# Kernel optimization log

Measured on AMD Instinct MI355X. Metric: run time of the kernel, lower is better.

## Reference

```python
import jax, jax.numpy as jnp
import numpy as np

D_MODEL = 2048
NUM_HEADS = 16
HEAD_DIM = D_MODEL // NUM_HEADS
SCALE = HEAD_DIM ** 0.5
B, TQ, CACHE_LEN = 4, 1024, 1024


def setup_inputs() -> dict:
    key = jax.random.key(0)
    ks = jax.random.split(key, 13)
    f = jnp.float32
    inp = {
        'query': jax.random.normal(ks[0], (B, TQ, D_MODEL), f),
        'key': jax.random.normal(ks[1], (B, TQ, D_MODEL), f),
        'value': jax.random.normal(ks[2], (B, TQ, D_MODEL), f),
        'cache_key': jax.random.normal(ks[3], (B, CACHE_LEN, D_MODEL), f),
        'cache_value': jax.random.normal(ks[4], (B, CACHE_LEN, D_MODEL), f),
        'Wq': jax.random.normal(ks[5], (D_MODEL, D_MODEL), f) * 0.02,
        'bq': jnp.zeros((D_MODEL,), f),
        'Wk': jax.random.normal(ks[6], (D_MODEL, D_MODEL), f) * 0.02,
        'bk': jnp.zeros((D_MODEL,), f),
        'Wv': jax.random.normal(ks[7], (D_MODEL, D_MODEL), f) * 0.02,
        'bv': jnp.zeros((D_MODEL,), f),
        'Wo': jax.random.normal(ks[8], (D_MODEL, D_MODEL), f) * 0.02,
        'bo': jnp.zeros((D_MODEL,), f),
    }
    return inp


def _split(x):
    b, t, _ = x.shape
    return jnp.transpose(x.reshape(b, t, NUM_HEADS, HEAD_DIM), (0, 2, 1, 3))  # [B,H,T,Dh]


def reference(query, key, value, cache_key, cache_value, Wq, bq, Wk, bk, Wv, bv, Wo, bo):
    b, tq, _ = query.shape
    Q = query @ Wq.T + bq
    K = key @ Wk.T + bk
    V = value @ Wv.T + bv
    # cache holds already-projected K/V; concat along time
    K = jnp.concatenate([cache_key, K], axis=1)
    V = jnp.concatenate([cache_value, V], axis=1)
    total = K.shape[1]
    Qh, Kh, Vh = _split(Q), _split(K), _split(V)  # [B,H,T,Dh]
    scores = jnp.einsum('bhqd,bhkd->bhqk', Qh, Kh) / SCALE  # [B,H,Tq,total]
    # faithful to original: tril(Tq, total) mask (row i sees cols 0..i)
    mask = jnp.tril(jnp.ones((tq, total), dtype=bool))
    scores = jnp.where(mask[None, None], scores, -jnp.inf)
    attn = jax.nn.softmax(scores, axis=-1)  # eval mode: no dropout
    out = jnp.einsum('bhqk,bhkd->bhqd', attn, Vh)
    out = jnp.transpose(out, (0, 2, 1, 3)).reshape(b, tq, D_MODEL)
    out = out @ Wo.T + bo
    # new cache: torch reshapes the transposed [B,H,T,Dh] tensor directly
    new_k = Kh.reshape(b, -1, D_MODEL)
    new_v = Vh.reshape(b, -1, D_MODEL)
    return out, new_k, new_v
```

## Files before the change

### kernel.cpp

```cpp
#include <hip/hip_runtime.h>
#include <hip/hip_bf16.h>


typedef __bf16 bf16x8 __attribute__((ext_vector_type(8)));
typedef __bf16 bf16x4 __attribute__((ext_vector_type(4)));
typedef unsigned short u16x8 __attribute__((ext_vector_type(8)));
typedef float  f32x4  __attribute__((ext_vector_type(4)));
typedef unsigned int u32;

#define MFMA16(a, b, c) __builtin_amdgcn_mfma_f32_16x16x32_bf16((a), (b), (c), 0, 0, 0)

__device__ __forceinline__ void async16(__bf16* lds, const __bf16* g) {
    __builtin_amdgcn_global_load_lds(
        (__attribute__((address_space(1))) void*)g,
        (__attribute__((address_space(3))) void*)lds, 16, 0, 0);
}

__global__ __launch_bounds__(256) void cvt_all(
    const float* __restrict__ q, const float* __restrict__ k, const float* __restrict__ v,
    const float* __restrict__ wq, const float* __restrict__ wk,
    const float* __restrict__ wv, const float* __restrict__ wo,
    __bf16* __restrict__ dq, __bf16* __restrict__ dk, __bf16* __restrict__ dv,
    __bf16* __restrict__ dwq, __bf16* __restrict__ dwk,
    __bf16* __restrict__ dwv, __bf16* __restrict__ dwo) {
    const int nthreads = gridDim.x * blockDim.x;
    for (int i = blockIdx.x * blockDim.x + threadIdx.x; i < 5242880; i += nthreads) {
        const float* s;
        __bf16* d;
        int off;
        if (i < (3 << 20)) {
            const int r = i >> 20;
            off = i & ((1 << 20) - 1);
            s = (r == 0) ? q : (r == 1) ? k : v;
            d = (r == 0) ? dq : (r == 1) ? dk : dv;
        } else {
            const int j = i - (3 << 20);
            const int r = j >> 19;
            off = j & ((1 << 19) - 1);
            s = (r == 0) ? wq : (r == 1) ? wk : (r == 2) ? wv : wo;
            d = (r == 0) ? dwq : (r == 1) ? dwk : (r == 2) ? dwv : dwo;
        }
        const f32x4 x0 = *(const f32x4*)(s + (size_t)off * 8);
        const f32x4 x1 = *(const f32x4*)(s + (size_t)off * 8 + 4);
        bf16x8 o;
#pragma unroll
        for (int j = 0; j < 4; j++) {
            o[j]     = (__bf16)x0[j];
            o[j + 4] = (__bf16)x1[j];
        }
        *(bf16x8*)(d + (size_t)off * 8) = o;
    }
}

template <int MODE>
__global__ __launch_bounds__(256) void gemm_bf(const __bf16* __restrict__ A,
                                               const __bf16* __restrict__ W,
                                               const float* __restrict__ bias,
                                               void* __restrict__ Cv) {
    constexpr int K = 2048;
    __shared__ __bf16 aT[128 * 32];
    __shared__ __bf16 bT[128 * 32];

    float* Cf = (float*)Cv;
    __bf16* Cb = (__bf16*)Cv;

    const int tid = threadIdx.x;
    const int w = tid >> 6;
    const int lane = tid & 63;

    const int lin = (blockIdx.y << 4) | blockIdx.x;
    const int swz = ((lin & 7) << 6) | (lin >> 3);
    const int m0 = (swz >> 4) << 7;
    const int n0 = (swz & 15) << 7;

    const int wr = w >> 1, wc = w & 1;
    const int g = lane >> 4, c = lane & 15;

    const int srow = w * 32 + (lane >> 2);
    const int kch = (lane & 3) * 8;
    const __bf16* gA0 = A + (size_t)(m0 + srow) * K + kch;
    const __bf16* gB0 = W + (size_t)(n0 + srow) * K + kch;
    __bf16* lA0 = &aT[w * 1024];
    __bf16* lB0 = &bT[w * 1024];

    f32x4 acc[4][4] = {};
    const int arow = wr * 64 + c;
    const int brow = wc * 64 + c;
    const int koff = g * 8;

    for (int k0 = 0; k0 < K; k0 += 32) {
        async16(lA0,       gA0 + k0);
        async16(lA0 + 512, gA0 + 16 * K + k0);
        async16(lB0,       gB0 + k0);
        async16(lB0 + 512, gB0 + 16 * K + k0);
        __syncthreads();
        bf16x8 af[4], bfr[4];
#pragma unroll
        for (int t = 0; t < 4; t++) {
            af[t]  = *(const bf16x8*)&aT[(arow + t * 16) * 32 + koff];
            bfr[t] = *(const bf16x8*)&bT[(brow + t * 16) * 32 + koff];
        }
#pragma unroll
        for (int ti = 0; ti < 4; ti++)
#pragma unroll
            for (int tj = 0; tj < 4; tj++)
                acc[ti][tj] = MFMA16(af[ti], bfr[tj], acc[ti][tj]);
        __syncthreads();
    }

#pragma unroll
    for (int tj = 0; tj < 4; tj++) {
        const int gcol = n0 + wc * 64 + tj * 16 + c;
        const float bv = bias[gcol];
#pragma unroll
        for (int ti = 0; ti < 4; ti++) {
            const int growb = m0 + wr * 64 + ti * 16 + g * 4;
#pragma unroll
            for (int r = 0; r < 4; r++) {
                const float v = acc[ti][tj][r] + bv;
                const int row = growb + r;
                if (MODE == 0) {
                    Cf[(size_t)row * 2048 + gcol] = v;
                } else {
                    const int b = row >> 10, t = row & 1023;
                    const int h = gcol >> 7, dh = gcol & 127;
                    if (MODE == 1)
                        Cb[(((size_t)(b * 16 + h) * 1024) + t) * 128 + dh] = (__bf16)v;
                    else
                        Cf[(((size_t)(b * 16 + h) * 2048) + 1024 + t) * 128 + dh] = v;
                }
            }
        }
    }
}

__global__ __launch_bounds__(256) void copy_cache(const float* __restrict__ ck,
                                                  const float* __restrict__ cv,
                                                  float* __restrict__ nk,
                                                  float* __restrict__ nv,
                                                  __bf16* __restrict__ ckb,
                                                  __bf16* __restrict__ cvb) {
    const int nthreads = gridDim.x * blockDim.x;
    for (int i = blockIdx.x * blockDim.x + threadIdx.x; i < 4194304; i += nthreads) {
        const int sel = i >> 21;
        const int j = i & 2097151;
        const int dh4 = j & 31;
        const int t = (j >> 5) & 1023;
        const int h = (j >> 15) & 15;
        const int b = j >> 19;
        const float* src = sel ? cv : ck;
        float* dst = sel ? nv : nk;
        __bf16* dstb = sel ? cvb : ckb;
        const size_t si = ((size_t)(b << 10) + t) * 2048 + (h << 7) + (dh4 << 2);
        const size_t di = ((size_t)b << 22) + ((size_t)h << 18) + (t << 7) + (dh4 << 2);
        const f32x4 x = *(const f32x4*)&src[si];
        *(f32x4*)&dst[di] = x;
        bf16x4 bx;
#pragma unroll
        for (int e = 0; e < 4; e++) bx[e] = (__bf16)x[e];
        *(bf16x4*)&dstb[si] = bx;
    }
}

__global__ __launch_bounds__(256) void attn_k(const __bf16* __restrict__ Qw,
                                              const __bf16* __restrict__ cK,
                                              const __bf16* __restrict__ cV,
                                              __bf16* __restrict__ O) {
    __shared__ __bf16 Kt[32 * 128];
    __shared__ u32 Vt32[128 * 16];
    __shared__ __bf16 Pw[4][16 * 32];

    const int tid = threadIdx.x;
    const int w = tid >> 6;
    const int lane = tid & 63;
    const int g = lane >> 4, c = lane & 15;

    const int lin = blockIdx.x + (blockIdx.y << 4) + (blockIdx.z << 8);
    const int chunk = lin >> 8, idx = lin & 255;
    int qb = idx & 15;
    if (chunk & 1) qb = 15 - qb;
    const int bh = (idx >> 4) + (chunk << 4);
    const int b = bh >> 4, h = bh & 15;
    const int q0 = qb << 6;
    const float inv_scale = 0.08838834764831845f;

    const __bf16* qbase = Qw + (((size_t)(b * 16 + h) * 1024) + q0 + w * 16) * 128;
    bf16x8 qf[4];
#pragma unroll
    for (int dc = 0; dc < 4; dc++)
        qf[dc] = *(const bf16x8*)&qbase[c * 128 + dc * 32 + g * 8];

    f32x4 accO[8] = {};
    float m_run[4], l_run[4];
#pragma unroll
    for (int r = 0; r < 4; r++) { m_run[r] = -1e30f; l_run[r] = 0.0f; }

    const int trips = (q0 >> 5) + 2;
    const __bf16* kb = cK + (size_t)b * 1024 * 2048 + h * 128;
    const __bf16* vb = cV + (size_t)b * 1024 * 2048 + h * 128;

    const int skey = tid >> 3, sdh = (tid & 7) * 16;
    const int kp = tid >> 4, db = tid & 15;
    const int vcol = (((kp >> 2) ^ (db & 3)) << 2) | (kp & 3);

    for (int kt = 0; kt < trips; kt++) {
        const int k0 = kt * 32;
        const bf16x8 k_lo = *(const bf16x8*)&kb[(size_t)(k0 + skey) * 2048 + sdh];
        const bf16x8 k_hi = *(const bf16x8*)&kb[(size_t)(k0 + skey) * 2048 + sdh + 8];
        const bf16x8 v0 = *(const bf16x8*)&vb[(size_t)(k0 + 2 * kp) * 2048 + db * 8];
        const bf16x8 v1 = *(const bf16x8*)&vb[(size_t)(k0 + 2 * kp + 1) * 2048 + db * 8];
        __syncthreads();
        {
            const int ss = skey & 7, ch0 = (tid & 7) * 2;
            *(bf16x8*)&Kt[skey * 128 + ((ch0 ^ ss) << 3)]       = k_lo;
            *(bf16x8*)&Kt[skey * 128 + (((ch0 + 1) ^ ss) << 3)] = k_hi;
        }
        {
            const u16x8 pa = __builtin_bit_cast(u16x8, v0);
            const u16x8 pb = __builtin_bit_cast(u16x8, v1);
#pragma unroll
            for (int j = 0; j < 8; j++)
                Vt32[(db * 8 + j) * 16 + vcol] = (u32)pa[j] | ((u32)pb[j] << 16);
        }
        __syncthreads();

        f32x4 s_acc[2] = {};
#pragma unroll
        for (int nt = 0; nt < 2; nt++) {
            const int krow = nt * 16 + c;
            const int ks = krow & 7;
#pragma unroll
            for (int dc = 0; dc < 4; dc++) {
                const bf16x8 kf =
                    *(const bf16x8*)&Kt[krow * 128 + (((dc * 4 + g) ^ ks) << 3)];
                s_acc[nt] = MFMA16(qf[dc], kf, s_acc[nt]);
            }
        }

        float p[2][4], alpha[4];
#pragma unroll
        for (int r = 0; r < 4; r++) {
            const int qrow = q0 + w * 16 + g * 4 + r;
            float s0 = (k0 + c      <= qrow) ? s_acc[0][r] * inv_scale : -1e30f;
            float s1 = (k0 + 16 + c <= qrow) ? s_acc[1][r] * inv_scale : -1e30f;
            float rm = fmaxf(s0, s1);
            rm = fmaxf(rm, __shfl_xor(rm, 1));
            rm = fmaxf(rm, __shfl_xor(rm, 2));
            rm = fmaxf(rm, __shfl_xor(rm, 4));
            rm = fmaxf(rm, __shfl_xor(rm, 8));
            const float mnew = fmaxf(m_run[r], rm);
            alpha[r] = __expf(m_run[r] - mnew);
            const float p0 = __expf(s0 - mnew);
            const float p1 = __expf(s1 - mnew);
            p[0][r] = p0; p[1][r] = p1;
            float ps = p0 + p1;
            ps += __shfl_xor(ps, 1);
            ps += __shfl_xor(ps, 2);
            ps += __shfl_xor(ps, 4);
            ps += __shfl_xor(ps, 8);
            l_run[r] = alpha[r] * l_run[r] + ps;
            m_run[r] = mnew;
        }
#pragma unroll
        for (int nt2 = 0; nt2 < 8; nt2++)
#pragma unroll
            for (int r = 0; r < 4; r++)
                accO[nt2][r] *= alpha[r];

#pragma unroll
        for (int nt = 0; nt < 2; nt++)
#pragma unroll
            for (int r = 0; r < 4; r++)
                Pw[w][(g * 4 + r) * 32 + ((((nt << 1) | (c >> 3)) ^ g) << 3) + (c & 7)] =
                    (__bf16)p[nt][r];
        __syncthreads();

        const bf16x8 pf = *(const bf16x8*)&Pw[w][c * 32 + ((g ^ ((c >> 2) & 3)) << 3)];
#pragma unroll
        for (int nt2 = 0; nt2 < 8; nt2++) {
            const int vrow = nt2 * 16 + c;
            const bf16x8 vf = *(const bf16x8*)&(
                (const __bf16*)Vt32)[vrow * 32 + ((g ^ ((vrow >> 3) & 3)) << 3)];
            accO[nt2] = MFMA16(pf, vf, accO[nt2]);
        }
    }

#pragma unroll
    for (int nt2 = 0; nt2 < 8; nt2++)
#pragma unroll
        for (int r = 0; r < 4; r++) {
            const float v = accO[nt2][r] / l_run[r];
            const int row = b * 1024 + q0 + w * 16 + g * 4 + r;
            const int col = h * 128 + nt2 * 16 + c;
            O[(size_t)row * 2048 + col] = (__bf16)v;
        }
}

extern "C" void kernel_launch(void* const* d_in, const int* in_sizes, int n_in,
                              void* d_out, int out_size, void* d_ws, size_t ws_size,
                              hipStream_t stream) {
    const float* query       = (const float*)d_in[0];
    const float* key         = (const float*)d_in[1];
    const float* value       = (const float*)d_in[2];
    const float* cache_key   = (const float*)d_in[3];
    const float* cache_value = (const float*)d_in[4];
    const float* Wq = (const float*)d_in[5];
    const float* bq = (const float*)d_in[6];
    const float* Wk = (const float*)d_in[7];
    const float* bk = (const float*)d_in[8];
    const float* Wv = (const float*)d_in[9];
    const float* bv = (const float*)d_in[10];
    const float* Wo = (const float*)d_in[11];
    const float* bo = (const float*)d_in[12];

    float* out   = (float*)d_out;
    float* new_k = out + 8388608;
    float* new_v = out + 25165824;

    __bf16* p = (__bf16*)d_ws;
    __bf16* ws_q    = p; p += 8388608;
    __bf16* ws_attn = p; p += 8388608;
    __bf16* q_bf    = p; p += 8388608;
    __bf16* k_bf    = p; p += 8388608;
    __bf16* v_bf    = p; p += 8388608;
    __bf16* wq_bf   = p; p += 4194304;
    __bf16* wk_bf   = p; p += 4194304;
    __bf16* wv_bf   = p; p += 4194304;
    __bf16* wo_bf   = p; p += 4194304;
    __bf16* ck_bf   = p; p += 8388608;
    __bf16* cv_bf   = p;

    const dim3 gemm_grid(16, 32);

    copy_cache<<<4096, 256, 0, stream>>>(cache_key, cache_value, new_k, new_v,
                                         ck_bf, cv_bf);
    cvt_all<<<2048, 256, 0, stream>>>(query, key, value, Wq, Wk, Wv, Wo,
                                      q_bf, k_bf, v_bf, wq_bf, wk_bf, wv_bf, wo_bf);
    gemm_bf<1><<<gemm_grid, 256, 0, stream>>>(q_bf, wq_bf, bq, ws_q);
    gemm_bf<2><<<gemm_grid, 256, 0, stream>>>(k_bf, wk_bf, bk, new_k);
    gemm_bf<2><<<gemm_grid, 256, 0, stream>>>(v_bf, wv_bf, bv, new_v);
    attn_k<<<dim3(16, 16, 4), 256, 0, stream>>>(ws_q, ck_bf, cv_bf, ws_attn);
    gemm_bf<0><<<gemm_grid, 256, 0, stream>>>(ws_attn, wo_bf, bo, out);
}
```

Baseline: 650.6 us.

## Fuse prep kernels, batch QKV GEMMs, widen attention key tile

The cache copy and the fp32-to-bf16 conversion kernels are merged into one prep kernel, which now also writes the bf16 cache in head-major layout. The three QKV projection GEMMs become a single launch that picks its weight, bias and output per row segment; this relies on q_bf, k_bf and v_bf sitting contiguously in the workspace. The attention kernel moves to 64-key tiles, loads K asynchronously straight into LDS from the contiguous head-major cache, and replaces the block barrier before the per-wave P buffer read with an LDS waitcnt. The aim is fewer launches, better GPU fill and fewer barriers, at the cost of more LDS per block and a dependence on workspace layout.

```diff
diff --git a/kernel.cpp b/kernel.cpp
--- a/kernel.cpp
+++ b/kernel.cpp
@@ -16,62 +16,90 @@
         (__attribute__((address_space(3))) void*)lds, 16, 0, 0);
 }
 
-__global__ __launch_bounds__(256) void cvt_all(
+__global__ __launch_bounds__(256) void prep(
     const float* __restrict__ q, const float* __restrict__ k, const float* __restrict__ v,
     const float* __restrict__ wq, const float* __restrict__ wk,
     const float* __restrict__ wv, const float* __restrict__ wo,
+    const float* __restrict__ ck, const float* __restrict__ cv,
+    float* __restrict__ nk, float* __restrict__ nv,
     __bf16* __restrict__ dq, __bf16* __restrict__ dk, __bf16* __restrict__ dv,
     __bf16* __restrict__ dwq, __bf16* __restrict__ dwk,
-    __bf16* __restrict__ dwv, __bf16* __restrict__ dwo) {
+    __bf16* __restrict__ dwv, __bf16* __restrict__ dwo,
+    __bf16* __restrict__ ckb, __bf16* __restrict__ cvb) {
     const int nthreads = gridDim.x * blockDim.x;
-    for (int i = blockIdx.x * blockDim.x + threadIdx.x; i < 5242880; i += nthreads) {
-        const float* s;
-        __bf16* d;
-        int off;
-        if (i < (3 << 20)) {
-            const int r = i >> 20;
-            off = i & ((1 << 20) - 1);
-            s = (r == 0) ? q : (r == 1) ? k : v;
-            d = (r == 0) ? dq : (r == 1) ? dk : dv;
+    for (int i = blockIdx.x * blockDim.x + threadIdx.x; i < 9437184; i += nthreads) {
+        if (i < 4194304) {
+            const int sel = i >> 21;
+            const int j = i & 2097151;
+            const int dh4 = j & 31;
+            const int t = (j >> 5) & 1023;
+            const int h = (j >> 15) & 15;
+            const int b = j >> 19;
+            const float* src = sel ? cv : ck;
+            float* dst = sel ? nv : nk;
+            __bf16* dstb = sel ? cvb : ckb;
+            const size_t si = ((size_t)(b << 10) + t) * 2048 + (h << 7) + (dh4 << 2);
+            const size_t di = ((size_t)b << 22) + ((size_t)h << 18) + (t << 7) + (dh4 << 2);
+            const size_t bi = (((size_t)(b * 16 + h) * 1024 + t) << 7) + (dh4 << 2);
+            const f32x4 x = *(const f32x4*)&src[si];
+            *(f32x4*)&dst[di] = x;
+            bf16x4 bx;
+#pragma unroll
+            for (int e = 0; e < 4; e++) bx[e] = (__bf16)x[e];
+            *(bf16x4*)&dstb[bi] = bx;
         } else {
-            const int j = i - (3 << 20);
-            const int r = j >> 19;
-            off = j & ((1 << 19) - 1);
-            s = (r == 0) ? wq : (r == 1) ? wk : (r == 2) ? wv : wo;
-            d = (r == 0) ? dwq : (r == 1) ? dwk : (r == 2) ? dwv : dwo;
-        }
-        const f32x4 x0 = *(const f32x4*)(s + (size_t)off * 8);
-        const f32x4 x1 = *(const f32x4*)(s + (size_t)off * 8 + 4);
-        bf16x8 o;
-#pragma unroll
-        for (int j = 0; j < 4; j++) {
-            o[j]     = (__bf16)x0[j];
-            o[j + 4] = (__bf16)x1[j];
-        }
-        *(bf16x8*)(d + (size_t)off * 8) = o;
-    }
-}
-
-template <int MODE>
-__global__ __launch_bounds__(256) void gemm_bf(const __bf16* __restrict__ A,
-                                               const __bf16* __restrict__ W,
-                                               const float* __restrict__ bias,
-                                               void* __restrict__ Cv) {
+            const float* s;
+            __bf16* d;
+            int off;
+            if (i < 7340032) {
+                const int ii = i - 4194304;
+                const int r = ii >> 20;
+                off = ii & 1048575;
+                s = (r == 0) ? q : (r == 1) ? k : v;
+                d = (r == 0) ? dq : (r == 1) ? dk : dv;
+            } else {
+                const int ii = i - 7340032;
+                const int r = ii >> 19;
+                off = ii & 524287;
+                s = (r == 0) ? wq : (r == 1) ? wk : (r == 2) ? wv : wo;
+                d = (r == 0) ? dwq : (r == 1) ? dwk : (r == 2) ? dwv : dwo;
+            }
+            const f32x4 x0 = *(const f32x4*)(s + (size_t)off * 8);
+            const f32x4 x1 = *(const f32x4*)(s + (size_t)off * 8 + 4);
+            bf16x8 o;
+#pragma unroll
+            for (int j2 = 0; j2 < 4; j2++) {
+                o[j2]     = (__bf16)x0[j2];
+                o[j2 + 4] = (__bf16)x1[j2];
+            }
+            *(bf16x8*)(d + (size_t)off * 8) = o;
+        }
+    }
+}
+
+__global__ __launch_bounds__(256) void gemm_qkv(
+    const __bf16* __restrict__ A,
+    const __bf16* __restrict__ Wqb, const __bf16* __restrict__ Wkb,
+    const __bf16* __restrict__ Wvb,
+    const float* __restrict__ bq, const float* __restrict__ bk,
+    const float* __restrict__ bv,
+    __bf16* __restrict__ ws_q, float* __restrict__ new_k,
+    float* __restrict__ new_v) {
     constexpr int K = 2048;
     __shared__ __bf16 aT[128 * 32];
     __shared__ __bf16 bT[128 * 32];
 
-    float* Cf = (float*)Cv;
-    __bf16* Cb = (__bf16*)Cv;
-
     const int tid = threadIdx.x;
     const int w = tid >> 6;
     const int lane = tid & 63;
 
     const int lin = (blockIdx.y << 4) | blockIdx.x;
-    const int swz = ((lin & 7) << 6) | (lin >> 3);
-    const int m0 = (swz >> 4) << 7;
-    const int n0 = (swz & 15) << 7;
+    const int swz = (lin & 7) * 192 + (lin >> 3);
+    const int mb = swz >> 4, nb = swz & 15;
+    const int m0 = mb << 7, n0 = nb << 7;
+    const int seg = mb >> 5;
+    const __bf16* W = (seg == 0) ? Wqb : (seg == 1) ? Wkb : Wvb;
+    const float* bias = (seg == 0) ? bq : (seg == 1) ? bk : bv;
 
     const int wr = w >> 1, wc = w & 1;
     const int g = lane >> 4, c = lane & 15;
@@ -111,54 +139,90 @@
 #pragma unroll
     for (int tj = 0; tj < 4; tj++) {
         const int gcol = n0 + wc * 64 + tj * 16 + c;
-        const float bv = bias[gcol];
+        const float bv2 = bias[gcol];
+        const int h = gcol >> 7, dh = gcol & 127;
 #pragma unroll
         for (int ti = 0; ti < 4; ti++) {
             const int growb = m0 + wr * 64 + ti * 16 + g * 4;
 #pragma unroll
             for (int r = 0; r < 4; r++) {
-                const float v = acc[ti][tj][r] + bv;
-                const int row = growb + r;
-                if (MODE == 0) {
-                    Cf[(size_t)row * 2048 + gcol] = v;
-                } else {
-                    const int b = row >> 10, t = row & 1023;
-                    const int h = gcol >> 7, dh = gcol & 127;
-                    if (MODE == 1)
-                        Cb[(((size_t)(b * 16 + h) * 1024) + t) * 128 + dh] = (__bf16)v;
-                    else
-                        Cf[(((size_t)(b * 16 + h) * 2048) + 1024 + t) * 128 + dh] = v;
-                }
-            }
-        }
-    }
-}
-
-__global__ __launch_bounds__(256) void copy_cache(const float* __restrict__ ck,
-                                                  const float* __restrict__ cv,
-                                                  float* __restrict__ nk,
-                                                  float* __restrict__ nv,
-                                                  __bf16* __restrict__ ckb,
-                                                  __bf16* __restrict__ cvb) {
-    const int nthreads = gridDim.x * blockDim.x;
-    for (int i = blockIdx.x * blockDim.x + threadIdx.x; i < 4194304; i += nthreads) {
-        const int sel = i >> 21;
-        const int j = i & 2097151;
-        const int dh4 = j & 31;
-        const int t = (j >> 5) & 1023;
-        const int h = (j >> 15) & 15;
-        const int b = j >> 19;
-        const float* src = sel ? cv : ck;
-        float* dst = sel ? nv : nk;
-        __bf16* dstb = sel ? cvb : ckb;
-        const size_t si = ((size_t)(b << 10) + t) * 2048 + (h << 7) + (dh4 << 2);
-        const size_t di = ((size_t)b << 22) + ((size_t)h << 18) + (t << 7) + (dh4 << 2);
-        const f32x4 x = *(const f32x4*)&src[si];
-        *(f32x4*)&dst[di] = x;
-        bf16x4 bx;
-#pragma unroll
-        for (int e = 0; e < 4; e++) bx[e] = (__bf16)x[e];
-        *(bf16x4*)&dstb[si] = bx;
+                const float vv = acc[ti][tj][r] + bv2;
+                const int lrow = (growb + r) - (seg << 12);
+                const int b = lrow >> 10, t = lrow & 1023;
+                if (seg == 0)
+                    ws_q[(((size_t)(b * 16 + h) * 1024) + t) * 128 + dh] = (__bf16)vv;
+                else if (seg == 1)
+                    new_k[(((size_t)(b * 16 + h) * 2048) + 1024 + t) * 128 + dh] = vv;
+                else
+                    new_v[(((size_t)(b * 16 + h) * 2048) + 1024 + t) * 128 + dh] = vv;
+            }
+        }
+    }
+}
+
+__global__ __launch_bounds__(256) void gemm_o(const __bf16* __restrict__ A,
+                                              const __bf16* __restrict__ W,
+                                              const float* __restrict__ bias,
+                                              float* __restrict__ C) {
+    constexpr int K = 2048;
+    __shared__ __bf16 aT[128 * 32];
+    __shared__ __bf16 bT[128 * 32];
+
+    const int tid = threadIdx.x;
+    const int w = tid >> 6;
+    const int lane = tid & 63;
+
+    const int lin = (blockIdx.y << 4) | blockIdx.x;
+    const int swz = ((lin & 7) << 6) | (lin >> 3);
+    const int m0 = (swz >> 4) << 7;
+    const int n0 = (swz & 15) << 7;
+
+    const int wr = w >> 1, wc = w & 1;
+    const int g = lane >> 4, c = lane & 15;
+
+    const int srow = w * 32 + (lane >> 2);
+    const int kch = (lane & 3) * 8;
+    const __bf16* gA0 = A + (size_t)(m0 + srow) * K + kch;
+    const __bf16* gB0 = W + (size_t)(n0 + srow) * K + kch;
+    __bf16* lA0 = &aT[w * 1024];
+    __bf16* lB0 = &bT[w * 1024];
+
+    f32x4 acc[4][4] = {};
+    const int arow = wr * 64 + c;
+    const int brow = wc * 64 + c;
+    const int koff = g * 8;
+
+    for (int k0 = 0; k0 < K; k0 += 32) {
+        async16(lA0,       gA0 + k0);
+        async16(lA0 + 512, gA0 + 16 * K + k0);
+        async16(lB0,       gB0 + k0);
+        async16(lB0 + 512, gB0 + 16 * K + k0);
+        __syncthreads();
+        bf16x8 af[4], bfr[4];
+#pragma unroll
+        for (int t = 0; t < 4; t++) {
+            af[t]  = *(const bf16x8*)&aT[(arow + t * 16) * 32 + koff];
+            bfr[t] = *(const bf16x8*)&bT[(brow + t * 16) * 32 + koff];
+        }
+#pragma unroll
+        for (int ti = 0; ti < 4; ti++)
+#pragma unroll
+            for (int tj = 0; tj < 4; tj++)
+                acc[ti][tj] = MFMA16(af[ti], bfr[tj], acc[ti][tj]);
+        __syncthreads();
+    }
+
+#pragma unroll
+    for (int tj = 0; tj < 4; tj++) {
+        const int gcol = n0 + wc * 64 + tj * 16 + c;
+        const float bv = bias[gcol];
+#pragma unroll
+        for (int ti = 0; ti < 4; ti++) {
+            const int growb = m0 + wr * 64 + ti * 16 + g * 4;
+#pragma unroll
+            for (int r = 0; r < 4; r++)
+                C[(size_t)(growb + r) * 2048 + gcol] = acc[ti][tj][r] + bv;
+        }
     }
 }
 
@@ -166,9 +230,9 @@
                                               const __bf16* __restrict__ cK,
                                               const __bf16* __restrict__ cV,
                                               __bf16* __restrict__ O) {
-    __shared__ __bf16 Kt[32 * 128];
-    __shared__ u32 Vt32[128 * 16];
-    __shared__ __bf16 Pw[4][16 * 32];
+    __shared__ __bf16 Kt[64 * 128];
+    __shared__ u32    Vt32[128 * 32];
+    __shared__ __bf16 Pw[4][16 * 64];
 
     const int tid = threadIdx.x;
     const int w = tid >> 6;
@@ -176,10 +240,10 @@
     const int g = lane >> 4, c = lane & 15;
 
     const int lin = blockIdx.x + (blockIdx.y << 4) + (blockIdx.z << 8);
-    const int chunk = lin >> 8, idx = lin & 255;
-    int qb = idx & 15;
-    if (chunk & 1) qb = 15 - qb;
-    const int bh = (idx >> 4) + (chunk << 4);
+    const int bh = (lin & 7) | (((lin >> 3) & 7) << 3);
+    const int qraw = (lin >> 6) & 15;
+    const int tt = qraw >> 2;
+    const int qb = (tt == 1 || tt == 2) ? 15 - qraw : qraw;
     const int b = bh >> 4, h = bh & 15;
     const int q0 = qb << 6;
     const float inv_scale = 0.08838834764831845f;
@@ -195,38 +259,56 @@
 #pragma unroll
     for (int r = 0; r < 4; r++) { m_run[r] = -1e30f; l_run[r] = 0.0f; }
 
-    const int trips = (q0 >> 5) + 2;
-    const __bf16* kb = cK + (size_t)b * 1024 * 2048 + h * 128;
-    const __bf16* vb = cV + (size_t)b * 1024 * 2048 + h * 128;
-
-    const int skey = tid >> 3, sdh = (tid & 7) * 16;
-    const int kp = tid >> 4, db = tid & 15;
-    const int vcol = (((kp >> 2) ^ (db & 3)) << 2) | (kp & 3);
+    const int trips = qb + 1;
+    const __bf16* kb = cK + (size_t)(b * 16 + h) * 1024 * 128;
+    const __bf16* vb = cV + (size_t)(b * 16 + h) * 1024 * 128;
+
+    const int chl = lane & 15;
+    size_t ksrc[4];
+    __bf16* kdst[4];
+#pragma unroll
+    for (int j = 0; j < 4; j++) {
+        const int key = w * 16 + j * 4 + (lane >> 4);
+        ksrc[j] = (size_t)key * 128 + ((chl ^ (key & 7)) << 3);
+        kdst[j] = &Kt[(w * 16 + j * 4) * 128];
+    }
+
+    const int kp = ((tid & 7) << 2) | ((tid >> 3) & 3);
+    const int db = tid >> 5;
+    const __bf16* vbase = vb + (size_t)(2 * kp) * 128 + db * 16;
 
     for (int kt = 0; kt < trips; kt++) {
-        const int k0 = kt * 32;
-        const bf16x8 k_lo = *(const bf16x8*)&kb[(size_t)(k0 + skey) * 2048 + sdh];
-        const bf16x8 k_hi = *(const bf16x8*)&kb[(size_t)(k0 + skey) * 2048 + sdh + 8];
-        const bf16x8 v0 = *(const bf16x8*)&vb[(size_t)(k0 + 2 * kp) * 2048 + db * 8];
-        const bf16x8 v1 = *(const bf16x8*)&vb[(size_t)(k0 + 2 * kp + 1) * 2048 + db * 8];
-        __syncthreads();
+        const int k0 = kt * 64;
+        const __bf16* vr = vbase + (size_t)k0 * 128;
+        const bf16x8 v0a = *(const bf16x8*)&vr[0];
+        const bf16x8 v0b = *(const bf16x8*)&vr[8];
+        const bf16x8 v1a = *(const bf16x8*)&vr[128];
+        const bf16x8 v1b = *(const bf16x8*)&vr[136];
+        __syncthreads();
+#pragma unroll
+        for (int j = 0; j < 4; j++)
+            async16(kdst[j], kb + (size_t)k0 * 128 + ksrc[j]);
         {
-            const int ss = skey & 7, ch0 = (tid & 7) * 2;
-            *(bf16x8*)&Kt[skey * 128 + ((ch0 ^ ss) << 3)]       = k_lo;
-            *(bf16x8*)&Kt[skey * 128 + (((ch0 + 1) ^ ss) << 3)] = k_hi;
-        }
-        {
-            const u16x8 pa = __builtin_bit_cast(u16x8, v0);
-            const u16x8 pb = __builtin_bit_cast(u16x8, v1);
+            const u16x8 a0 = __builtin_bit_cast(u16x8, v0a);
+            const u16x8 a1 = __builtin_bit_cast(u16x8, v0b);
+            const u16x8 b0 = __builtin_bit_cast(u16x8, v1a);
+            const u16x8 b1 = __builtin_bit_cast(u16x8, v1b);
+            const int colhi = kp & 3;
+            const int kph = kp >> 2;
 #pragma unroll
             for (int j = 0; j < 8; j++)
-                Vt32[(db * 8 + j) * 16 + vcol] = (u32)pa[j] | ((u32)pb[j] << 16);
-        }
-        __syncthreads();
-
-        f32x4 s_acc[2] = {};
-#pragma unroll
-        for (int nt = 0; nt < 2; nt++) {
+                Vt32[(db * 16 + j) * 32 + ((kph ^ j) << 2) + colhi] =
+                    (u32)a0[j] | ((u32)b0[j] << 16);
+#pragma unroll
+            for (int j = 0; j < 8; j++)
+                Vt32[(db * 16 + 8 + j) * 32 + ((kph ^ j) << 2) + colhi] =
+                    (u32)a1[j] | ((u32)b1[j] << 16);
+        }
+        __syncthreads();
+
+        f32x4 s_acc[4] = {};
+#pragma unroll
+        for (int nt = 0; nt < 4; nt++) {
             const int krow = nt * 16 + c;
             const int ks = krow & 7;
 #pragma unroll
@@ -237,23 +319,27 @@
             }
         }
 
-        float p[2][4], alpha[4];
+        float p[4][4], alpha[4];
 #pragma unroll
         for (int r = 0; r < 4; r++) {
             const int qrow = q0 + w * 16 + g * 4 + r;
-            float s0 = (k0 + c      <= qrow) ? s_acc[0][r] * inv_scale : -1e30f;
-            float s1 = (k0 + 16 + c <= qrow) ? s_acc[1][r] * inv_scale : -1e30f;
-            float rm = fmaxf(s0, s1);
+            float s[4];
+#pragma unroll
+            for (int nt = 0; nt < 4; nt++)
+                s[nt] = (k0 + nt * 16 + c <= qrow) ? s_acc[nt][r] * inv_scale : -1e30f;
+            float rm = fmaxf(fmaxf(s[0], s[1]), fmaxf(s[2], s[3]));
             rm = fmaxf(rm, __shfl_xor(rm, 1));
             rm = fmaxf(rm, __shfl_xor(rm, 2));
             rm = fmaxf(rm, __shfl_xor(rm, 4));
             rm = fmaxf(rm, __shfl_xor(rm, 8));
             const float mnew = fmaxf(m_run[r], rm);
             alpha[r] = __expf(m_run[r] - mnew);
-            const float p0 = __expf(s0 - mnew);
-            const float p1 = __expf(s1 - mnew);
-            p[0][r] = p0; p[1][r] = p1;
-            float ps = p0 + p1;
+            float ps = 0.0f;
+#pragma unroll
+            for (int nt = 0; nt < 4; nt++) {
+                p[nt][r] = __expf(s[nt] - mnew);
+                ps += p[nt][r];
+            }
             ps += __shfl_xor(ps, 1);
             ps += __shfl_xor(ps, 2);
             ps += __shfl_xor(ps, 4);
@@ -268,20 +354,29 @@
                 accO[nt2][r] *= alpha[r];
 
 #pragma unroll
-        for (int nt = 0; nt < 2; nt++)
-#pragma unroll
-            for (int r = 0; r < 4; r++)
-                Pw[w][(g * 4 + r) * 32 + ((((nt << 1) | (c >> 3)) ^ g) << 3) + (c & 7)] =
-                    (__bf16)p[nt][r];
-        __syncthreads();
-
-        const bf16x8 pf = *(const bf16x8*)&Pw[w][c * 32 + ((g ^ ((c >> 2) & 3)) << 3)];
+        for (int nt = 0; nt < 4; nt++)
+#pragma unroll
+            for (int r = 0; r < 4; r++) {
+                const int row = g * 4 + r;
+                const int cc = (nt * 2 + (c >> 3)) ^ (row & 7);
+                Pw[w][row * 64 + (cc << 3) + (c & 7)] = (__bf16)p[nt][r];
+            }
+        asm volatile("s_waitcnt lgkmcnt(0)" ::: "memory");
+        __builtin_amdgcn_sched_barrier(0);
+
+        bf16x8 pf[2];
+#pragma unroll
+        for (int s2 = 0; s2 < 2; s2++)
+            pf[s2] = *(const bf16x8*)&Pw[w][c * 64 + (((s2 * 4 + g) ^ (c & 7)) << 3)];
 #pragma unroll
         for (int nt2 = 0; nt2 < 8; nt2++) {
-            const int vrow = nt2 * 16 + c;
-            const bf16x8 vf = *(const bf16x8*)&(
-                (const __bf16*)Vt32)[vrow * 32 + ((g ^ ((vrow >> 3) & 3)) << 3)];
-            accO[nt2] = MFMA16(pf, vf, accO[nt2]);
+            const int d = nt2 * 16 + c;
+#pragma unroll
+            for (int s2 = 0; s2 < 2; s2++) {
+                const bf16x8 vf = *(const bf16x8*)&Vt32[d * 32 +
+                    (((s2 * 4 + g) ^ (d & 7)) << 2)];
+                accO[nt2] = MFMA16(pf[s2], vf, accO[nt2]);
+            }
         }
     }
 
@@ -330,15 +425,12 @@
     __bf16* ck_bf   = p; p += 8388608;
     __bf16* cv_bf   = p;
 
-    const dim3 gemm_grid(16, 32);
-
-    copy_cache<<<4096, 256, 0, stream>>>(cache_key, cache_value, new_k, new_v,
-                                         ck_bf, cv_bf);
-    cvt_all<<<2048, 256, 0, stream>>>(query, key, value, Wq, Wk, Wv, Wo,
-                                      q_bf, k_bf, v_bf, wq_bf, wk_bf, wv_bf, wo_bf);
-    gemm_bf<1><<<gemm_grid, 256, 0, stream>>>(q_bf, wq_bf, bq, ws_q);
-    gemm_bf<2><<<gemm_grid, 256, 0, stream>>>(k_bf, wk_bf, bk, new_k);
-    gemm_bf<2><<<gemm_grid, 256, 0, stream>>>(v_bf, wv_bf, bv, new_v);
+    prep<<<4096, 256, 0, stream>>>(query, key, value, Wq, Wk, Wv, Wo,
+                                   cache_key, cache_value, new_k, new_v,
+                                   q_bf, k_bf, v_bf, wq_bf, wk_bf, wv_bf, wo_bf,
+                                   ck_bf, cv_bf);
+    gemm_qkv<<<dim3(16, 96), 256, 0, stream>>>(q_bf, wq_bf, wk_bf, wv_bf,
+                                               bq, bk, bv, ws_q, new_k, new_v);
     attn_k<<<dim3(16, 16, 4), 256, 0, stream>>>(ws_q, ck_bf, cv_bf, ws_attn);
-    gemm_bf<0><<<gemm_grid, 256, 0, stream>>>(ws_attn, wo_bf, bo, out);
-}
+    gemm_o<<<dim3(16, 32), 256, 0, stream>>>(ws_attn, wo_bf, bo, out);
+}
```

After: 671.7 us. +3.2%, slower.

## Replace GEMMs with 256x256 double-buffered 8-wave kernel and fuse prep kernels

Applied to the files above, without the earlier changes.

Replaces the 128x128 single-buffered GEMM with a 256x256-tile, 512-thread kernel that double-buffers LDS through async global-to-LDS loads. MFMA phases are interleaved with explicit barriers and setprio. The three Q/K/V projections become one launch over stacked rows, relying on q_bf/k_bf/v_bf being contiguous. The cache copy and conversion kernels merge into one prep kernel that writes the bf16 cache in head-major layout so attention reads contiguous rows. A workgroup barrier in attention is replaced with an lgkmcnt wait, since the P tile is per-wave. Risks include high LDS use (128KB) limiting occupancy and only 128 blocks for the output GEMM.

```diff
diff --git a/kernel.cpp b/kernel.cpp
--- a/kernel.cpp
+++ b/kernel.cpp
@@ -10,155 +10,230 @@
 
 #define MFMA16(a, b, c) __builtin_amdgcn_mfma_f32_16x16x32_bf16((a), (b), (c), 0, 0, 0)
 
-__device__ __forceinline__ void async16(__bf16* lds, const __bf16* g) {
+__device__ __forceinline__ void async16(__bf16* lds_p, const __bf16* g) {
     __builtin_amdgcn_global_load_lds(
         (__attribute__((address_space(1))) void*)g,
-        (__attribute__((address_space(3))) void*)lds, 16, 0, 0);
+        (__attribute__((address_space(3))) void*)lds_p, 16, 0, 0);
 }
 
-__global__ __launch_bounds__(256) void cvt_all(
+__global__ __launch_bounds__(256) void prep(
     const float* __restrict__ q, const float* __restrict__ k, const float* __restrict__ v,
     const float* __restrict__ wq, const float* __restrict__ wk,
     const float* __restrict__ wv, const float* __restrict__ wo,
+    const float* __restrict__ ck, const float* __restrict__ cv,
+    float* __restrict__ nk, float* __restrict__ nv,
     __bf16* __restrict__ dq, __bf16* __restrict__ dk, __bf16* __restrict__ dv,
     __bf16* __restrict__ dwq, __bf16* __restrict__ dwk,
-    __bf16* __restrict__ dwv, __bf16* __restrict__ dwo) {
+    __bf16* __restrict__ dwv, __bf16* __restrict__ dwo,
+    __bf16* __restrict__ ckb, __bf16* __restrict__ cvb) {
     const int nthreads = gridDim.x * blockDim.x;
-    for (int i = blockIdx.x * blockDim.x + threadIdx.x; i < 5242880; i += nthreads) {
-        const float* s;
-        __bf16* d;
-        int off;
-        if (i < (3 << 20)) {
-            const int r = i >> 20;
-            off = i & ((1 << 20) - 1);
-            s = (r == 0) ? q : (r == 1) ? k : v;
-            d = (r == 0) ? dq : (r == 1) ? dk : dv;
+    for (int i = blockIdx.x * blockDim.x + threadIdx.x; i < 9437184; i += nthreads) {
+        if (i < 4194304) {
+            const int sel = i >> 21;
+            const int j = i & 2097151;
+            const int dh4 = j & 31;
+            const int t = (j >> 5) & 1023;
+            const int h = (j >> 15) & 15;
+            const int b = j >> 19;
+            const float* src = sel ? cv : ck;
+            float* dst = sel ? nv : nk;
+            __bf16* dstb = sel ? cvb : ckb;
+            const size_t si = ((size_t)(b << 10) + t) * 2048 + (h << 7) + (dh4 << 2);
+            const size_t di = ((size_t)b << 22) + ((size_t)h << 18) + (t << 7) + (dh4 << 2);
+            const size_t bi = (((size_t)(b * 16 + h) * 1024 + t) << 7) + (dh4 << 2);
+            const f32x4 x = *(const f32x4*)&src[si];
+            *(f32x4*)&dst[di] = x;
+            bf16x4 bx;
+#pragma unroll
+            for (int e = 0; e < 4; e++) bx[e] = (__bf16)x[e];
+            *(bf16x4*)&dstb[bi] = bx;
         } else {
-            const int j = i - (3 << 20);
-            const int r = j >> 19;
-            off = j & ((1 << 19) - 1);
-            s = (r == 0) ? wq : (r == 1) ? wk : (r == 2) ? wv : wo;
-            d = (r == 0) ? dwq : (r == 1) ? dwk : (r == 2) ? dwv : dwo;
-        }
-        const f32x4 x0 = *(const f32x4*)(s + (size_t)off * 8);
-        const f32x4 x1 = *(const f32x4*)(s + (size_t)off * 8 + 4);
-        bf16x8 o;
-#pragma unroll
-        for (int j = 0; j < 4; j++) {
-            o[j]     = (__bf16)x0[j];
-            o[j + 4] = (__bf16)x1[j];
-        }
-        *(bf16x8*)(d + (size_t)off * 8) = o;
+            const float* s;
+            __bf16* d;
+            int off;
+            if (i < 7340032) {
+                const int ii = i - 4194304;
+                const int r = ii >> 20;
+                off = ii & 1048575;
+                s = (r == 0) ? q : (r == 1) ? k : v;
+                d = (r == 0) ? dq : (r == 1) ? dk : dv;
+            } else {
+                const int ii = i - 7340032;
+                const int r = ii >> 19;
+                off = ii & 524287;
+                s = (r == 0) ? wq : (r == 1) ? wk : (r == 2) ? wv : wo;
+                d = (r == 0) ? dwq : (r == 1) ? dwk : (r == 2) ? dwv : dwo;
+            }
+            const f32x4 x0 = *(const f32x4*)(s + (size_t)off * 8);
+            const f32x4 x1 = *(const f32x4*)(s + (size_t)off * 8 + 4);
+            bf16x8 o;
+#pragma unroll
+            for (int j2 = 0; j2 < 4; j2++) {
+                o[j2]     = (__bf16)x0[j2];
+                o[j2 + 4] = (__bf16)x1[j2];
+            }
+            *(bf16x8*)(d + (size_t)off * 8) = o;
+        }
     }
 }
 
 template <int MODE>
-__global__ __launch_bounds__(256) void gemm_bf(const __bf16* __restrict__ A,
-                                               const __bf16* __restrict__ W,
-                                               const float* __restrict__ bias,
-                                               void* __restrict__ Cv) {
+__global__ __launch_bounds__(512, 2) void gemm8(
+    const __bf16* __restrict__ A,
+    const __bf16* __restrict__ W0, const __bf16* __restrict__ W1,
+    const __bf16* __restrict__ W2,
+    const float* __restrict__ bz0, const float* __restrict__ bz1,
+    const float* __restrict__ bz2,
+    void* __restrict__ C0, float* __restrict__ C1, float* __restrict__ C2) {
+    extern __shared__ __bf16 lds[];
     constexpr int K = 2048;
-    __shared__ __bf16 aT[128 * 32];
-    __shared__ __bf16 bT[128 * 32];
-
-    float* Cf = (float*)Cv;
-    __bf16* Cb = (__bf16*)Cv;
-
     const int tid = threadIdx.x;
-    const int w = tid >> 6;
-    const int lane = tid & 63;
-
-    const int lin = (blockIdx.y << 4) | blockIdx.x;
-    const int swz = ((lin & 7) << 6) | (lin >> 3);
-    const int m0 = (swz >> 4) << 7;
-    const int n0 = (swz & 15) << 7;
-
-    const int wr = w >> 1, wc = w & 1;
+    const int w = tid >> 6, lane = tid & 63;
+    const int wm = w >> 2, wn = w & 3;
     const int g = lane >> 4, c = lane & 15;
 
-    const int srow = w * 32 + (lane >> 2);
-    const int kch = (lane & 3) * 8;
-    const __bf16* gA0 = A + (size_t)(m0 + srow) * K + kch;
-    const __bf16* gB0 = W + (size_t)(n0 + srow) * K + kch;
-    __bf16* lA0 = &aT[w * 1024];
-    __bf16* lB0 = &bT[w * 1024];
-
-    f32x4 acc[4][4] = {};
-    const int arow = wr * 64 + c;
-    const int brow = wc * 64 + c;
-    const int koff = g * 8;
-
-    for (int k0 = 0; k0 < K; k0 += 32) {
-        async16(lA0,       gA0 + k0);
-        async16(lA0 + 512, gA0 + 16 * K + k0);
-        async16(lB0,       gB0 + k0);
-        async16(lB0 + 512, gB0 + 16 * K + k0);
-        __syncthreads();
-        bf16x8 af[4], bfr[4];
-#pragma unroll
-        for (int t = 0; t < 4; t++) {
-            af[t]  = *(const bf16x8*)&aT[(arow + t * 16) * 32 + koff];
-            bfr[t] = *(const bf16x8*)&bT[(brow + t * 16) * 32 + koff];
-        }
-#pragma unroll
-        for (int ti = 0; ti < 4; ti++)
-#pragma unroll
-            for (int tj = 0; tj < 4; tj++)
-                acc[ti][tj] = MFMA16(af[ti], bfr[tj], acc[ti][tj]);
-        __syncthreads();
+    const int lin = blockIdx.x;
+    const int nb = lin & 7, mb = lin >> 3;
+    const int m0 = mb << 8, n0 = nb << 8;
+    const int seg = (MODE == 1) ? (mb >> 4) : 0;
+    const __bf16* W = (MODE == 0 || seg == 0) ? W0 : (seg == 1) ? W1 : W2;
+    const float* bias = (MODE == 0) ? bz0 : (seg == 0) ? bz0 : (seg == 1) ? bz1 : bz2;
+
+    const __bf16* Ab = A + (size_t)m0 * K;
+    const __bf16* Wb = W + (size_t)n0 * K;
+
+    const int sch = (lane & 3) ^ (((lane >> 5) & 1) << 1);
+    const int srow = lane >> 2;
+    const int foff = c * 32 + ((g ^ ((c >> 3) << 1)) << 3);
+    const int arow0 = wm * 8;
+    const int brow0 = wn * 4;
+
+    f32x4 acc[8][4] = {};
+
+    auto stg = [&](const __bf16* src, int T, int kk, int region, int bf) {
+#pragma unroll
+        for (int cc = 0; cc < 2; cc++) {
+            const __bf16* gs = src + (size_t)((cc * 8 + w) * 16 + srow) * K
+                             + T * 64 + kk * 32 + sch * 8;
+            async16(&lds[bf * 32768 + region * 16384 + kk * 8192 + (cc * 8 + w) * 512], gs);
+        }
+    };
+
+    stg(Ab, 0, 0, 0, 0); stg(Wb, 0, 0, 1, 0);
+    stg(Ab, 0, 1, 0, 0); stg(Wb, 0, 1, 1, 0);
+    stg(Ab, 1, 0, 0, 1); stg(Wb, 1, 0, 1, 1);
+    stg(Ab, 1, 1, 0, 1); stg(Wb, 1, 1, 1, 1);
+    asm volatile("s_waitcnt vmcnt(0)" ::: "memory");
+    asm volatile("s_barrier" ::: "memory");
+
+#pragma unroll 2
+    for (int T = 0; T < 32; T++) {
+        const int bf = T & 1;
+        const int ab = bf * 32768;
+        const int bb = bf * 32768 + 16384;
+        bf16x8 fa[4], fb[4], fb2[4];
+
+#pragma unroll
+        for (int i = 0; i < 4; i++)
+            fa[i] = *(const bf16x8*)&lds[ab + (arow0 + i) * 512 + foff];
+#pragma unroll
+        for (int j = 0; j < 4; j++)
+            fb[j] = *(const bf16x8*)&lds[bb + (brow0 + j) * 512 + foff];
+        if (T >= 1 && T <= 30) stg(Ab, T + 1, 1, 0, bf ^ 1);
+        asm volatile("s_barrier" ::: "memory");
+        asm volatile("s_waitcnt lgkmcnt(0)" ::: "memory");
+        __builtin_amdgcn_sched_barrier(0);
+        __builtin_amdgcn_s_setprio(1);
+#pragma unroll
+        for (int i = 0; i < 4; i++)
+#pragma unroll
+            for (int j = 0; j < 4; j++)
+                acc[i][j] = MFMA16(fa[i], fb[j], acc[i][j]);
+        __builtin_amdgcn_s_setprio(0);
+        asm volatile("s_barrier" ::: "memory");
+
+#pragma unroll
+        for (int i = 0; i < 4; i++)
+            fa[i] = *(const bf16x8*)&lds[ab + (arow0 + 4 + i) * 512 + foff];
+        if (T >= 1 && T <= 30) stg(Wb, T + 1, 1, 1, bf ^ 1);
+        asm volatile("s_barrier" ::: "memory");
+        asm volatile("s_waitcnt lgkmcnt(0)" ::: "memory");
+        __builtin_amdgcn_sched_barrier(0);
+        __builtin_amdgcn_s_setprio(1);
+#pragma unroll
+        for (int i = 0; i < 4; i++)
+#pragma unroll
+            for (int j = 0; j < 4; j++)
+                acc[4 + i][j] = MFMA16(fa[i], fb[j], acc[4 + i][j]);
+        __builtin_amdgcn_s_setprio(0);
+        asm volatile("s_barrier" ::: "memory");
+
+#pragma unroll
+        for (int i = 0; i < 4; i++)
+            fa[i] = *(const bf16x8*)&lds[ab + 8192 + (arow0 + i) * 512 + foff];
+#pragma unroll
+        for (int j = 0; j < 4; j++)
+            fb2[j] = *(const bf16x8*)&lds[bb + 8192 + (brow0 + j) * 512 + foff];
+        if (T <= 29) stg(Ab, T + 2, 0, 0, bf);
+        asm volatile("s_barrier" ::: "memory");
+        asm volatile("s_waitcnt lgkmcnt(0)" ::: "memory");
+        __builtin_amdgcn_sched_barrier(0);
+        __builtin_amdgcn_s_setprio(1);
+#pragma unroll
+        for (int i = 0; i < 4; i++)
+#pragma unroll
+            for (int j = 0; j < 4; j++)
+                acc[i][j] = MFMA16(fa[i], fb2[j], acc[i][j]);
+        __builtin_amdgcn_s_setprio(0);
+        asm volatile("s_barrier" ::: "memory");
+
+#pragma unroll
+        for (int i = 0; i < 4; i++)
+            fa[i] = *(const bf16x8*)&lds[ab + 8192 + (arow0 + 4 + i) * 512 + foff];
+        if (T <= 29) stg(Wb, T + 2, 0, 1, bf);
+        if (T >= 30) asm volatile("s_waitcnt vmcnt(0)" ::: "memory");
+        else         asm volatile("s_waitcnt vmcnt(4)" ::: "memory");
+        asm volatile("s_barrier" ::: "memory");
+        asm volatile("s_waitcnt lgkmcnt(0)" ::: "memory");
+        __builtin_amdgcn_sched_barrier(0);
+        __builtin_amdgcn_s_setprio(1);
+#pragma unroll
+        for (int i = 0; i < 4; i++)
+#pragma unroll
+            for (int j = 0; j < 4; j++)
+                acc[4 + i][j] = MFMA16(fa[i], fb2[j], acc[4 + i][j]);
+        __builtin_amdgcn_s_setprio(0);
+        asm volatile("s_barrier" ::: "memory");
     }
 
 #pragma unroll
-    for (int tj = 0; tj < 4; tj++) {
-        const int gcol = n0 + wc * 64 + tj * 16 + c;
-        const float bv = bias[gcol];
-#pragma unroll
-        for (int ti = 0; ti < 4; ti++) {
-            const int growb = m0 + wr * 64 + ti * 16 + g * 4;
-#pragma unroll
-            for (int r = 0; r < 4; r++) {
-                const float v = acc[ti][tj][r] + bv;
-                const int row = growb + r;
-                if (MODE == 0) {
-                    Cf[(size_t)row * 2048 + gcol] = v;
-                } else {
-                    const int b = row >> 10, t = row & 1023;
-                    const int h = gcol >> 7, dh = gcol & 127;
-                    if (MODE == 1)
-                        Cb[(((size_t)(b * 16 + h) * 1024) + t) * 128 + dh] = (__bf16)v;
+    for (int mi = 0; mi < 8; mi++) {
+#pragma unroll
+        for (int ni = 0; ni < 4; ni++) {
+            const int col = n0 + wn * 64 + ni * 16 + c;
+            const float bv = bias[col];
+            const int rowb = m0 + wm * 128 + mi * 16 + g * 4;
+            if (MODE == 0) {
+                float* Cf = (float*)C0;
+#pragma unroll
+                for (int r = 0; r < 4; r++)
+                    Cf[(size_t)(rowb + r) * 2048 + col] = acc[mi][ni][r] + bv;
+            } else {
+                const int h = col >> 7, dh = col & 127;
+#pragma unroll
+                for (int r = 0; r < 4; r++) {
+                    const float v = acc[mi][ni][r] + bv;
+                    const int lrow = (rowb + r) & 4095;
+                    const int b = lrow >> 10, t = lrow & 1023;
+                    if (seg == 0)
+                        ((__bf16*)C0)[(((size_t)(b * 16 + h) * 1024) + t) * 128 + dh] = (__bf16)v;
+                    else if (seg == 1)
+                        C1[(((size_t)(b * 16 + h) * 2048) + 1024 + t) * 128 + dh] = v;
                     else
-                        Cf[(((size_t)(b * 16 + h) * 2048) + 1024 + t) * 128 + dh] = v;
+                        C2[(((size_t)(b * 16 + h) * 2048) + 1024 + t) * 128 + dh] = v;
                 }
             }
         }
-    }
-}
-
-__global__ __launch_bounds__(256) void copy_cache(const float* __restrict__ ck,
-                                                  const float* __restrict__ cv,
-                                                  float* __restrict__ nk,
-                                                  float* __restrict__ nv,
-                                                  __bf16* __restrict__ ckb,
-                                                  __bf16* __restrict__ cvb) {
-    const int nthreads = gridDim.x * blockDim.x;
-    for (int i = blockIdx.x * blockDim.x + threadIdx.x; i < 4194304; i += nthreads) {
-        const int sel = i >> 21;
-        const int j = i & 2097151;
-        const int dh4 = j & 31;
-        const int t = (j >> 5) & 1023;
-        const int h = (j >> 15) & 15;
-        const int b = j >> 19;
-        const float* src = sel ? cv : ck;
-        float* dst = sel ? nv : nk;
-        __bf16* dstb = sel ? cvb : ckb;
-        const size_t si = ((size_t)(b << 10) + t) * 2048 + (h << 7) + (dh4 << 2);
-        const size_t di = ((size_t)b << 22) + ((size_t)h << 18) + (t << 7) + (dh4 << 2);
-        const f32x4 x = *(const f32x4*)&src[si];
-        *(f32x4*)&dst[di] = x;
-        bf16x4 bx;
-#pragma unroll
-        for (int e = 0; e < 4; e++) bx[e] = (__bf16)x[e];
-        *(bf16x4*)&dstb[si] = bx;
     }
 }
 
@@ -196,8 +271,8 @@
     for (int r = 0; r < 4; r++) { m_run[r] = -1e30f; l_run[r] = 0.0f; }
 
     const int trips = (q0 >> 5) + 2;
-    const __bf16* kb = cK + (size_t)b * 1024 * 2048 + h * 128;
-    const __bf16* vb = cV + (size_t)b * 1024 * 2048 + h * 128;
+    const __bf16* kb = cK + (size_t)(b * 16 + h) * 1024 * 128;
+    const __bf16* vb = cV + (size_t)(b * 16 + h) * 1024 * 128;
 
     const int skey = tid >> 3, sdh = (tid & 7) * 16;
     const int kp = tid >> 4, db = tid & 15;
@@ -205,10 +280,10 @@
 
     for (int kt = 0; kt < trips; kt++) {
         const int k0 = kt * 32;
-        const bf16x8 k_lo = *(const bf16x8*)&kb[(size_t)(k0 + skey) * 2048 + sdh];
-        const bf16x8 k_hi = *(const bf16x8*)&kb[(size_t)(k0 + skey) * 2048 + sdh + 8];
-        const bf16x8 v0 = *(const bf16x8*)&vb[(size_t)(k0 + 2 * kp) * 2048 + db * 8];
-        const bf16x8 v1 = *(const bf16x8*)&vb[(size_t)(k0 + 2 * kp + 1) * 2048 + db * 8];
+        const bf16x8 k_lo = *(const bf16x8*)&kb[(size_t)(k0 + skey) * 128 + sdh];
+        const bf16x8 k_hi = *(const bf16x8*)&kb[(size_t)(k0 + skey) * 128 + sdh + 8];
+        const bf16x8 v0 = *(const bf16x8*)&vb[(size_t)(k0 + 2 * kp) * 128 + db * 8];
+        const bf16x8 v1 = *(const bf16x8*)&vb[(size_t)(k0 + 2 * kp + 1) * 128 + db * 8];
         __syncthreads();
         {
             const int ss = skey & 7, ch0 = (tid & 7) * 2;
@@ -273,7 +348,8 @@
             for (int r = 0; r < 4; r++)
                 Pw[w][(g * 4 + r) * 32 + ((((nt << 1) | (c >> 3)) ^ g) << 3) + (c & 7)] =
                     (__bf16)p[nt][r];
-        __syncthreads();
+        asm volatile("s_waitcnt lgkmcnt(0)" ::: "memory");
+        __builtin_amdgcn_sched_barrier(0);
 
         const bf16x8 pf = *(const bf16x8*)&Pw[w][c * 32 + ((g ^ ((c >> 2) & 3)) << 3)];
 #pragma unroll
@@ -330,15 +406,22 @@
     __bf16* ck_bf   = p; p += 8388608;
     __bf16* cv_bf   = p;
 
-    const dim3 gemm_grid(16, 32);
-
-    copy_cache<<<4096, 256, 0, stream>>>(cache_key, cache_value, new_k, new_v,
-                                         ck_bf, cv_bf);
-    cvt_all<<<2048, 256, 0, stream>>>(query, key, value, Wq, Wk, Wv, Wo,
-                                      q_bf, k_bf, v_bf, wq_bf, wk_bf, wv_bf, wo_bf);
-    gemm_bf<1><<<gemm_grid, 256, 0, stream>>>(q_bf, wq_bf, bq, ws_q);
-    gemm_bf<2><<<gemm_grid, 256, 0, stream>>>(k_bf, wk_bf, bk, new_k);
-    gemm_bf<2><<<gemm_grid, 256, 0, stream>>>(v_bf, wv_bf, bv, new_v);
+    static bool s_attr = false;
+    if (!s_attr) {
+        hipFuncSetAttribute(reinterpret_cast<const void*>(&gemm8<1>),
+                            hipFuncAttributeMaxDynamicSharedMemorySize, 131072);
+        hipFuncSetAttribute(reinterpret_cast<const void*>(&gemm8<0>),
+                            hipFuncAttributeMaxDynamicSharedMemorySize, 131072);
+        s_attr = true;
+    }
+
+    prep<<<4096, 256, 0, stream>>>(query, key, value, Wq, Wk, Wv, Wo,
+                                   cache_key, cache_value, new_k, new_v,
+                                   q_bf, k_bf, v_bf, wq_bf, wk_bf, wv_bf, wo_bf,
+                                   ck_bf, cv_bf);
+    gemm8<1><<<384, 512, 131072, stream>>>(q_bf, wq_bf, wk_bf, wv_bf,
+                                           bq, bk, bv, ws_q, new_k, new_v);
     attn_k<<<dim3(16, 16, 4), 256, 0, stream>>>(ws_q, ck_bf, cv_bf, ws_attn);
-    gemm_bf<0><<<gemm_grid, 256, 0, stream>>>(ws_attn, wo_bf, bo, out);
+    gemm8<0><<<128, 512, 131072, stream>>>(ws_attn, wo_bf, nullptr, nullptr,
+                                           bo, nullptr, nullptr, out, nullptr, nullptr);
 }
```

Measured after the change: 640.4 us. No clear change (-1.6%).
